# Optimization experiments

Measured on AMD Instinct MI355X. Metric: run time of the kernel, lower is better.

## Reference

```python
import jax, jax.numpy as jnp
import numpy as np


def log_g(x):
    # Appendix B.3 of 'Were RNNs All We Needed?'
    return jnp.where(x >= 0, jnp.log(jax.nn.relu(x) + 0.5), -jax.nn.softplus(-x))


def parallel_scan_log(log_a, log_b):
    # h[0] = b[0]; h[i] = a[i]*h[i-1] + b[i], computed in log space along axis 1
    log_a_star = jnp.cumsum(log_a, axis=1)
    log_x0_plus_b_star = jax.lax.cumlogsumexp(log_b - log_a_star, axis=1)
    return jnp.exp(log_a_star + log_x0_plus_b_star)


def setup_inputs() -> dict:
    key = jax.random.key(0)
    B, T, D = 8, 4096, 1024
    k1, k2, k3, k4, k5 = jax.random.split(key, 5)
    scale = 1.0 / np.sqrt(D)
    return {
        "h_prev_layer": jax.random.normal(k1, (B, T, D), dtype=jnp.float32),
        "W_z": jax.random.uniform(k2, (D, D), jnp.float32, -scale, scale),
        "b_z": jax.random.uniform(k3, (D,), jnp.float32, -scale, scale),
        "W_h": jax.random.uniform(k4, (D, D), jnp.float32, -scale, scale),
        "b_h": jax.random.uniform(k5, (D,), jnp.float32, -scale, scale),
    }


def reference(h_prev_layer, W_z, b_z, W_h, b_h):
    k = jnp.einsum('btd,ed->bte', h_prev_layer, W_z) + b_z          # linear_z
    tilde_h = jnp.einsum('btd,ed->bte', h_prev_layer, W_h) + b_h    # linear_h
    log_z = -jax.nn.softplus(-k)
    log_one_minus_z = -jax.nn.softplus(k)
    log_tilde_h = log_g(tilde_h)
    return parallel_scan_log(log_one_minus_z, log_z + log_tilde_h)
```

## Files before the change

kernel.cpp:

```cpp
#include <hip/hip_runtime.h>
#include <hip/hip_fp16.h>

typedef float f32x4 __attribute__((ext_vector_type(4)));
typedef __bf16 bf16x8 __attribute__((ext_vector_type(8)));

#define BB_ 8
#define TT_ 4096
#define DD_ 1024
#define MM_ (BB_*TT_)
#define KK_ DD_

#define BM 128
#define BN 128
#define BK 32

#define NCH 64
#define LCH (TT_/NCH)

static __device__ __forceinline__ unsigned short f2bf_rn(float f) {
  unsigned int u = __float_as_uint(f);
  u += 0x7FFFu + ((u >> 16) & 1u);
  return (unsigned short)(u >> 16);
}

__global__ void cvt_f32_bf16(const float4* __restrict__ src,
                             ushort4* __restrict__ dst, int n4) {
  int stride = gridDim.x * blockDim.x;
  for (int i = blockIdx.x * blockDim.x + threadIdx.x; i < n4; i += stride) {
    float4 v = src[i];
    ushort4 o;
    o.x = f2bf_rn(v.x); o.y = f2bf_rn(v.y);
    o.z = f2bf_rn(v.z); o.w = f2bf_rn(v.w);
    dst[i] = o;
  }
}

__device__ __forceinline__ void gload_lds16(const void* g, void* l) {
  __builtin_amdgcn_global_load_lds(
      (const __attribute__((address_space(1))) void*)g,
      (__attribute__((address_space(3))) void*)l, 16, 0, 0);
}

__global__ __launch_bounds__(256) void gemm_fused(
    const unsigned short* __restrict__ Xb,
    const unsigned short* __restrict__ Wb,
    const float* __restrict__ bz, const float* __restrict__ bh,
    __half* __restrict__ Zb, __half* __restrict__ Gb)
{
  __shared__ __align__(16) unsigned short lA[BM * BK];
  __shared__ __align__(16) unsigned short lB[BN * BK];
  const int tid  = threadIdx.x;
  const int wave = tid >> 6;
  const int lane = tid & 63;
  const int m0 = blockIdx.x * BM;
  const int e0 = blockIdx.y * BN;
  const int wr = wave >> 1, wc = wave & 1;
  const int fr = lane & 15;
  const int kg = lane >> 4;

  f32x4 acc[4][4];
  #pragma unroll
  for (int i = 0; i < 4; i++)
    #pragma unroll
    for (int j = 0; j < 4; j++)
      acc[i][j] = (f32x4){0.f, 0.f, 0.f, 0.f};

  for (int kk = 0; kk < KK_; kk += BK) {
    #pragma unroll
    for (int it = 0; it < 2; ++it) {
      int il  = (wave * 2 + it) * 64 + lane;
      int row = il >> 2;
      int col = (il & 3) * 8;
      gload_lds16(Xb + (size_t)(m0 + row) * KK_ + kk + col,
                  lA + (size_t)(wave * 2 + it) * 512);
      gload_lds16(Wb + (size_t)(e0 + row) * KK_ + kk + col,
                  lB + (size_t)(wave * 2 + it) * 512);
    }
    __syncthreads();
    bf16x8 af[4], bfv[4];
    #pragma unroll
    for (int i = 0; i < 4; i++)
      af[i] = *reinterpret_cast<const bf16x8*>(&lA[(wr * 64 + i * 16 + fr) * BK + kg * 8]);
    #pragma unroll
    for (int j = 0; j < 4; j++)
      bfv[j] = *reinterpret_cast<const bf16x8*>(&lB[(wc * 64 + j * 16 + fr) * BK + kg * 8]);
    #pragma unroll
    for (int i = 0; i < 4; i++)
      #pragma unroll
      for (int j = 0; j < 4; j++)
        acc[i][j] = __builtin_amdgcn_mfma_f32_16x16x32_bf16(af[i], bfv[j], acc[i][j], 0, 0, 0);
    __syncthreads();
  }

  const bool isZ = (e0 < DD_);
  const float* bias = isZ ? bz : bh;
  __half* outp = isZ ? Zb : Gb;
  const int ec0 = isZ ? e0 : (e0 - DD_);
  #pragma unroll
  for (int j = 0; j < 4; j++) {
    int e = ec0 + wc * 64 + j * 16 + fr;
    float bv = bias[e];
    #pragma unroll
    for (int i = 0; i < 4; i++) {
      int mb = m0 + wr * 64 + i * 16 + kg * 4;
      f32x4 v = acc[i][j];
      #pragma unroll
      for (int r = 0; r < 4; r++) {
        float val = v[r] + bv;
        float res;
        if (isZ) {
          res = 1.0f / (1.0f + __expf(-val));
        } else {
          res = (val >= 0.0f) ? (val + 0.5f)
                              : (1.0f / (1.0f + __expf(-val)));
        }
        outp[(size_t)(mb + r) * DD_ + e] = __float2half(res);
      }
    }
  }
}

__global__ __launch_bounds__(256) void scan_partial(
    const ushort4* __restrict__ Z, const ushort4* __restrict__ G,
    float4* __restrict__ P, float4* __restrict__ Q) {
  const int d4 = threadIdx.x;
  const int c  = blockIdx.x;
  const int b  = blockIdx.y;
  size_t base = ((size_t)b * TT_ + (size_t)c * LCH) * (DD_ / 4) + d4;
  float p0=1.f,p1=1.f,p2=1.f,p3=1.f, q0=0.f,q1=0.f,q2=0.f,q3=0.f;
  for (int t = 0; t < LCH; ++t) {
    ushort4 uz = Z[base + (size_t)t * (DD_ / 4)];
    ushort4 ug = G[base + (size_t)t * (DD_ / 4)];
    float z, g, a;
    z = __half2float(__ushort_as_half(uz.x)); g = __half2float(__ushort_as_half(ug.x));
    a = 1.f - z; p0 *= a; q0 = fmaf(a, q0, z * g);
    z = __half2float(__ushort_as_half(uz.y)); g = __half2float(__ushort_as_half(ug.y));
    a = 1.f - z; p1 *= a; q1 = fmaf(a, q1, z * g);
    z = __half2float(__ushort_as_half(uz.z)); g = __half2float(__ushort_as_half(ug.z));
    a = 1.f - z; p2 *= a; q2 = fmaf(a, q2, z * g);
    z = __half2float(__ushort_as_half(uz.w)); g = __half2float(__ushort_as_half(ug.w));
    a = 1.f - z; p3 *= a; q3 = fmaf(a, q3, z * g);
  }
  size_t o = ((size_t)b * NCH + c) * (DD_ / 4) + d4;
  P[o] = make_float4(p0, p1, p2, p3);
  Q[o] = make_float4(q0, q1, q2, q3);
}

__global__ __launch_bounds__(256) void scan_combine(
    const float4* __restrict__ P, const float4* __restrict__ Q,
    float4* __restrict__ H) {
  const int d4 = threadIdx.x;
  const int b  = blockIdx.x;
  float4 h = make_float4(0.f, 0.f, 0.f, 0.f);
  for (int c = 0; c < NCH; ++c) {
    size_t o = ((size_t)b * NCH + c) * (DD_ / 4) + d4;
    H[o] = h;
    float4 p = P[o], q = Q[o];
    h.x = fmaf(p.x, h.x, q.x);
    h.y = fmaf(p.y, h.y, q.y);
    h.z = fmaf(p.z, h.z, q.z);
    h.w = fmaf(p.w, h.w, q.w);
  }
}

__global__ __launch_bounds__(256) void scan_apply(
    const ushort4* __restrict__ Z, const ushort4* __restrict__ G,
    const float4* __restrict__ H, float4* __restrict__ out) {
  const int d4 = threadIdx.x;
  const int c  = blockIdx.x;
  const int b  = blockIdx.y;
  float4 h = H[((size_t)b * NCH + c) * (DD_ / 4) + d4];
  size_t base = ((size_t)b * TT_ + (size_t)c * LCH) * (DD_ / 4) + d4;
  for (int t = 0; t < LCH; ++t) {
    ushort4 uz = Z[base + (size_t)t * (DD_ / 4)];
    ushort4 ug = G[base + (size_t)t * (DD_ / 4)];
    float z, g, a;
    z = __half2float(__ushort_as_half(uz.x)); g = __half2float(__ushort_as_half(ug.x));
    a = 1.f - z; h.x = fmaf(a, h.x, z * g);
    z = __half2float(__ushort_as_half(uz.y)); g = __half2float(__ushort_as_half(ug.y));
    a = 1.f - z; h.y = fmaf(a, h.y, z * g);
    z = __half2float(__ushort_as_half(uz.z)); g = __half2float(__ushort_as_half(ug.z));
    a = 1.f - z; h.z = fmaf(a, h.z, z * g);
    z = __half2float(__ushort_as_half(uz.w)); g = __half2float(__ushort_as_half(ug.w));
    a = 1.f - z; h.w = fmaf(a, h.w, z * g);
    out[base + (size_t)t * (DD_ / 4)] = h;
  }
}

extern "C" void kernel_launch(void* const* d_in, const int* in_sizes, int n_in,
                              void* d_out, int out_size, void* d_ws, size_t ws_size,
                              hipStream_t stream) {
  const float* X  = (const float*)d_in[0];
  const float* Wz = (const float*)d_in[1];
  const float* bz = (const float*)d_in[2];
  const float* Wh = (const float*)d_in[3];
  const float* bh = (const float*)d_in[4];
  float* out = (float*)d_out;

  const size_t szXb = (size_t)MM_ * DD_ * 2;
  const size_t szWb = (size_t)2 * DD_ * DD_ * 2;
  const size_t szZ  = (size_t)MM_ * DD_ * 2;
  const size_t szPQ = (size_t)BB_ * NCH * DD_ * 4;

  char* ws = (char*)d_ws;
  unsigned short *Xb, *Wb;
  __half *Zb, *Gb;
  const size_t needA = szXb + szWb + 2 * szZ + 3 * szPQ;
  if (ws_size >= needA) {
    Xb = (unsigned short*)ws;              ws += szXb;
    Wb = (unsigned short*)ws;              ws += szWb;
  } else {
    Xb = (unsigned short*)d_out;
    Wb = (unsigned short*)((char*)d_out + szXb);
  }
  Zb = (__half*)ws;  ws += szZ;
  Gb = (__half*)ws;  ws += szZ;
  float* P = (float*)ws;  ws += szPQ;
  float* Q = (float*)ws;  ws += szPQ;
  float* H = (float*)ws;

  cvt_f32_bf16<<<2048, 256, 0, stream>>>((const float4*)X, (ushort4*)Xb,
                                         (int)((size_t)MM_ * DD_ / 4));
  cvt_f32_bf16<<<512, 256, 0, stream>>>((const float4*)Wz, (ushort4*)Wb,
                                        DD_ * DD_ / 4);
  cvt_f32_bf16<<<512, 256, 0, stream>>>((const float4*)Wh,
                                        (ushort4*)(Wb + (size_t)DD_ * DD_),
                                        DD_ * DD_ / 4);
  dim3 gg(MM_ / BM, (2 * DD_) / BN);
  gemm_fused<<<gg, 256, 0, stream>>>(Xb, Wb, bz, bh, Zb, Gb);

  scan_partial<<<dim3(NCH, BB_), 256, 0, stream>>>((const ushort4*)Zb, (const ushort4*)Gb,
                                                   (float4*)P, (float4*)Q);
  scan_combine<<<BB_, 256, 0, stream>>>((const float4*)P, (const float4*)Q, (float4*)H);
  scan_apply<<<dim3(NCH, BB_), 256, 0, stream>>>((const ushort4*)Zb, (const ushort4*)Gb,
                                                 (const float4*)H, (float4*)out);
}
```

Baseline: 325.1 us.

## Double-buffer GEMM LDS tiles, swizzle block order, stage epilogue through LDS

The GEMM main loop now uses two LDS buffers, so the global-to-LDS loads for the next K tile are issued while MFMAs run on the current tile. This removes one barrier per iteration. The grid is flattened with a block-index swizzle that groups tiles sharing rows of X, aiming for better L2 reuse. The epilogue writes fp16 results into LDS first, then stores 16-byte coalesced rows to global memory instead of scattered 2-byte stores. This doubles LDS use to 32KB, which may reduce occupancy.

Measured after the change: 335.3 us. +3.1%, slower.

```diff
diff --git a/kernel.cpp b/kernel.cpp
--- a/kernel.cpp
+++ b/kernel.cpp
@@ -47,16 +47,26 @@
     const float* __restrict__ bz, const float* __restrict__ bh,
     __half* __restrict__ Zb, __half* __restrict__ Gb)
 {
-  __shared__ __align__(16) unsigned short lA[BM * BK];
-  __shared__ __align__(16) unsigned short lB[BN * BK];
+  __shared__ __align__(16) char smem[32768];
+  unsigned short* lA0 = (unsigned short*)(smem);
+  unsigned short* lB0 = (unsigned short*)(smem + 8192);
+  unsigned short* lA1 = (unsigned short*)(smem + 16384);
+  unsigned short* lB1 = (unsigned short*)(smem + 24576);
+
   const int tid  = threadIdx.x;
   const int wave = tid >> 6;
   const int lane = tid & 63;
-  const int m0 = blockIdx.x * BM;
-  const int e0 = blockIdx.y * BN;
+
+  int swz = (blockIdx.x & 7) * 512 + (blockIdx.x >> 3);
+  const int m0 = (swz >> 4) * BM;
+  const int e0 = (swz & 15) * BN;
+
   const int wr = wave >> 1, wc = wave & 1;
   const int fr = lane & 15;
   const int kg = lane >> 4;
+
+  const int il0 = (wave * 2 + 0) * 64 + lane;
+  const int il1 = (wave * 2 + 1) * 64 + lane;
 
   f32x4 acc[4][4];
   #pragma unroll
@@ -65,57 +75,96 @@
     for (int j = 0; j < 4; j++)
       acc[i][j] = (f32x4){0.f, 0.f, 0.f, 0.f};
 
-  for (int kk = 0; kk < KK_; kk += BK) {
-    #pragma unroll
-    for (int it = 0; it < 2; ++it) {
-      int il  = (wave * 2 + it) * 64 + lane;
-      int row = il >> 2;
-      int col = (il & 3) * 8;
-      gload_lds16(Xb + (size_t)(m0 + row) * KK_ + kk + col,
-                  lA + (size_t)(wave * 2 + it) * 512);
-      gload_lds16(Wb + (size_t)(e0 + row) * KK_ + kk + col,
-                  lB + (size_t)(wave * 2 + it) * 512);
-    }
+#define STAGE(dA, dB, kkv) do { \
+    gload_lds16(Xb + (size_t)(m0 + (il0 >> 2)) * KK_ + (kkv) + (il0 & 3) * 8, \
+                (dA) + (size_t)(wave * 2 + 0) * 512); \
+    gload_lds16(Wb + (size_t)(e0 + (il0 >> 2)) * KK_ + (kkv) + (il0 & 3) * 8, \
+                (dB) + (size_t)(wave * 2 + 0) * 512); \
+    gload_lds16(Xb + (size_t)(m0 + (il1 >> 2)) * KK_ + (kkv) + (il1 & 3) * 8, \
+                (dA) + (size_t)(wave * 2 + 1) * 512); \
+    gload_lds16(Wb + (size_t)(e0 + (il1 >> 2)) * KK_ + (kkv) + (il1 & 3) * 8, \
+                (dB) + (size_t)(wave * 2 + 1) * 512); \
+  } while (0)
+
+#define COMPUTE(sA, sB) do { \
+    bf16x8 af[4], bfv[4]; \
+    _Pragma("unroll") \
+    for (int i = 0; i < 4; i++) \
+      af[i] = *reinterpret_cast<const bf16x8*>(&(sA)[(wr * 64 + i * 16 + fr) * BK + kg * 8]); \
+    _Pragma("unroll") \
+    for (int j = 0; j < 4; j++) \
+      bfv[j] = *reinterpret_cast<const bf16x8*>(&(sB)[(wc * 64 + j * 16 + fr) * BK + kg * 8]); \
+    _Pragma("unroll") \
+    for (int i = 0; i < 4; i++) \
+      _Pragma("unroll") \
+      for (int j = 0; j < 4; j++) \
+        acc[i][j] = __builtin_amdgcn_mfma_f32_16x16x32_bf16(af[i], bfv[j], acc[i][j], 0, 0, 0); \
+  } while (0)
+
+  STAGE(lA0, lB0, 0);
+  __syncthreads();
+  int kk = BK;
+  #pragma unroll 1
+  for (int t = 0; t < 15; ++t) {
+    STAGE(lA1, lB1, kk);
+    COMPUTE(lA0, lB0);
     __syncthreads();
-    bf16x8 af[4], bfv[4];
-    #pragma unroll
-    for (int i = 0; i < 4; i++)
-      af[i] = *reinterpret_cast<const bf16x8*>(&lA[(wr * 64 + i * 16 + fr) * BK + kg * 8]);
-    #pragma unroll
-    for (int j = 0; j < 4; j++)
-      bfv[j] = *reinterpret_cast<const bf16x8*>(&lB[(wc * 64 + j * 16 + fr) * BK + kg * 8]);
-    #pragma unroll
-    for (int i = 0; i < 4; i++)
-      #pragma unroll
-      for (int j = 0; j < 4; j++)
-        acc[i][j] = __builtin_amdgcn_mfma_f32_16x16x32_bf16(af[i], bfv[j], acc[i][j], 0, 0, 0);
+    kk += BK;
+    STAGE(lA0, lB0, kk);
+    COMPUTE(lA1, lB1);
     __syncthreads();
-  }
+    kk += BK;
+  }
+  STAGE(lA1, lB1, 31 * BK);
+  COMPUTE(lA0, lB0);
+  __syncthreads();
+  COMPUTE(lA1, lB1);
+  __syncthreads();
+#undef STAGE
+#undef COMPUTE
 
   const bool isZ = (e0 < DD_);
   const float* bias = isZ ? bz : bh;
   __half* outp = isZ ? Zb : Gb;
   const int ec0 = isZ ? e0 : (e0 - DD_);
+
+  float bv[4];
   #pragma unroll
-  for (int j = 0; j < 4; j++) {
-    int e = ec0 + wc * 64 + j * 16 + fr;
-    float bv = bias[e];
+  for (int j = 0; j < 4; j++) bv[j] = bias[ec0 + wc * 64 + j * 16 + fr];
+
+  __half* eo = (__half*)smem;
+  const int sub  = lane & 7;
+  const int rowr = lane >> 3;
+
+  #pragma unroll
+  for (int p = 0; p < 2; ++p) {
     #pragma unroll
-    for (int i = 0; i < 4; i++) {
-      int mb = m0 + wr * 64 + i * 16 + kg * 4;
-      f32x4 v = acc[i][j];
+    for (int i2 = 0; i2 < 2; ++i2) {
+      const int i = p * 2 + i2;
       #pragma unroll
-      for (int r = 0; r < 4; r++) {
-        float val = v[r] + bv;
-        float res;
-        if (isZ) {
-          res = 1.0f / (1.0f + __expf(-val));
-        } else {
-          res = (val >= 0.0f) ? (val + 0.5f)
-                              : (1.0f / (1.0f + __expf(-val)));
+      for (int j = 0; j < 4; j++) {
+        #pragma unroll
+        for (int r = 0; r < 4; r++) {
+          float val = acc[i][j][r] + bv[j];
+          float res;
+          if (isZ) {
+            res = 1.0f / (1.0f + __expf(-val));
+          } else {
+            res = (val >= 0.0f) ? (val + 0.5f)
+                                : (1.0f / (1.0f + __expf(-val)));
+          }
+          eo[(size_t)wave * 2304 + (i2 * 16 + kg * 4 + r) * 72 + j * 16 + fr] =
+              __float2half(res);
         }
-        outp[(size_t)(mb + r) * DD_ + e] = __float2half(res);
       }
+    }
+    #pragma unroll
+    for (int q = 0; q < 4; ++q) {
+      const int rl = q * 8 + rowr;
+      uint4 v = *reinterpret_cast<const uint4*>(
+          &eo[(size_t)wave * 2304 + rl * 72 + sub * 8]);
+      const size_t rg = (size_t)(m0 + wr * 64 + p * 32 + rl);
+      *reinterpret_cast<uint4*>(&outp[rg * DD_ + ec0 + wc * 64 + sub * 8]) = v;
     }
   }
 }
@@ -226,8 +275,7 @@
   cvt_f32_bf16<<<512, 256, 0, stream>>>((const float4*)Wh,
                                         (ushort4*)(Wb + (size_t)DD_ * DD_),
                                         DD_ * DD_ / 4);
-  dim3 gg(MM_ / BM, (2 * DD_) / BN);
-  gemm_fused<<<gg, 256, 0, stream>>>(Xb, Wb, bz, bh, Zb, Gb);
+  gemm_fused<<<(MM_ / BM) * ((2 * DD_) / BN), 256, 0, stream>>>(Xb, Wb, bz, bh, Zb, Gb);
 
   scan_partial<<<dim3(NCH, BB_), 256, 0, stream>>>((const ushort4*)Zb, (const ushort4*)Gb,
                                                    (float4*)P, (float4*)Q);
```

## Rewrite fused GEMM with 256x256 tiles, double-buffered LDS pipeline and swizzled layout

Applied to the files above, without the earlier changes.

The bf16 GEMM moves from 128x128x32 tiles with 256 threads to 256x256x64 tiles with 512 threads. It double-buffers 128 KB of dynamic LDS, interleaving global-to-LDS loads with MFMA phases, and XOR-swizzles the LDS layout to avoid bank conflicts. Blocks are remapped so consecutive blocks share tiles for L2 reuse, and the epilogue stages results through LDS to emit coalesced 16-byte stores. The aim is to cut the GEMM's memory traffic and synchronization stalls, at the cost of higher register and LDS pressure and one block per CU's worth of LDS.

New measurement: 284.3 us. 1.14x faster.

```diff
diff --git a/kernel.cpp b/kernel.cpp
--- a/kernel.cpp
+++ b/kernel.cpp
@@ -9,10 +9,6 @@
 #define DD_ 1024
 #define MM_ (BB_*TT_)
 #define KK_ DD_
-
-#define BM 128
-#define BN 128
-#define BK 32
 
 #define NCH 64
 #define LCH (TT_/NCH)
@@ -41,81 +37,142 @@
       (__attribute__((address_space(3))) void*)l, 16, 0, 0);
 }
 
-__global__ __launch_bounds__(256) void gemm_fused(
+#define STA(q, nb_, kkh) gload_lds16(pXa + (q) * 65536 + (kkh), (nb_) + (q) * 8192 + wofs)
+#define STB(q, nb_, kkh) gload_lds16(pWb + (q) * 65536 + (kkh), (nb_) + 32768 + (q) * 8192 + wofs)
+
+#define PHASE(cb_, mh, kh, STAGEOPS, WAITOPS) do {                          \
+    const char* Ab_ = (cb_);                                                \
+    const char* Bb_ = (cb_) + 32768;                                        \
+    const int sk_ = (kh) ? sk1 : sk0;                                       \
+    bf16x8 af_[4];                                                          \
+    _Pragma("unroll")                                                       \
+    for (int ii = 0; ii < 4; ++ii)                                          \
+      af_[ii] = *reinterpret_cast<const bf16x8*>(                           \
+          Ab_ + rA7 + (mh) * 8192 + ii * 2048 + sk_);                       \
+    if ((mh) == 0) {                                                        \
+      _Pragma("unroll")                                                     \
+      for (int j = 0; j < 4; ++j)                                           \
+        bfv[j] = *reinterpret_cast<const bf16x8*>(                          \
+            Bb_ + rB7 + j * 2048 + sk_);                                    \
+    }                                                                       \
+    STAGEOPS;                                                               \
+    WAITOPS;                                                                \
+    __builtin_amdgcn_s_barrier();                                           \
+    asm volatile("s_waitcnt lgkmcnt(0)" ::: "memory");                      \
+    __builtin_amdgcn_sched_barrier(0);                                      \
+    __builtin_amdgcn_s_setprio(1);                                          \
+    _Pragma("unroll")                                                       \
+    for (int ii = 0; ii < 4; ++ii)                                          \
+      _Pragma("unroll")                                                     \
+      for (int j = 0; j < 4; ++j)                                           \
+        acc[(mh) * 4 + ii][j] = __builtin_amdgcn_mfma_f32_16x16x32_bf16(    \
+            af_[ii], bfv[j], acc[(mh) * 4 + ii][j], 0, 0, 0);               \
+    __builtin_amdgcn_s_setprio(0);                                          \
+    asm volatile("" ::: "memory");                                          \
+    __builtin_amdgcn_s_barrier();                                           \
+  } while (0)
+
+__global__ __launch_bounds__(512, 2) void gemm_fused(
     const unsigned short* __restrict__ Xb,
     const unsigned short* __restrict__ Wb,
     const float* __restrict__ bz, const float* __restrict__ bh,
     __half* __restrict__ Zb, __half* __restrict__ Gb)
 {
-  __shared__ __align__(16) unsigned short lA[BM * BK];
-  __shared__ __align__(16) unsigned short lB[BN * BK];
+  extern __shared__ __align__(16) char smem[];
   const int tid  = threadIdx.x;
   const int wave = tid >> 6;
   const int lane = tid & 63;
-  const int m0 = blockIdx.x * BM;
-  const int e0 = blockIdx.y * BN;
-  const int wr = wave >> 1, wc = wave & 1;
-  const int fr = lane & 15;
-  const int kg = lane >> 4;
-
-  f32x4 acc[4][4];
+  const int wm = wave >> 2, wn = wave & 3;
+  const int fr = lane & 15, kg = lane >> 4, fx = fr & 7;
+
+  int swz = (blockIdx.x & 7) * 128 + (blockIdx.x >> 3);
+  const int m0 = (swz >> 3) * 256;
+  const int e0 = (swz & 7) * 256;
+
+  const int arow = tid >> 3;
+  const int aslx = ((tid & 7) ^ (arow & 7)) * 8;
+  const unsigned short* pXa = Xb + (size_t)(m0 + arow) * KK_ + aslx;
+  const unsigned short* pWb = Wb + (size_t)(e0 + arow) * KK_ + aslx;
+  const int wofs = wave * 1024;
+
+  const int rA7 = (wm * 128 + fr) * 128;
+  const int rB7 = (wn * 64 + fr) * 128;
+  const int sk0 = (kg ^ fx) * 16;
+  const int sk1 = sk0 ^ 64;
+
+  f32x4 acc[8][4];
   #pragma unroll
-  for (int i = 0; i < 4; i++)
+  for (int i = 0; i < 8; i++)
     #pragma unroll
     for (int j = 0; j < 4; j++)
       acc[i][j] = (f32x4){0.f, 0.f, 0.f, 0.f};
-
-  for (int kk = 0; kk < KK_; kk += BK) {
-    #pragma unroll
-    for (int it = 0; it < 2; ++it) {
-      int il  = (wave * 2 + it) * 64 + lane;
-      int row = il >> 2;
-      int col = (il & 3) * 8;
-      gload_lds16(Xb + (size_t)(m0 + row) * KK_ + kk + col,
-                  lA + (size_t)(wave * 2 + it) * 512);
-      gload_lds16(Wb + (size_t)(e0 + row) * KK_ + kk + col,
-                  lB + (size_t)(wave * 2 + it) * 512);
-    }
-    __syncthreads();
-    bf16x8 af[4], bfv[4];
-    #pragma unroll
-    for (int i = 0; i < 4; i++)
-      af[i] = *reinterpret_cast<const bf16x8*>(&lA[(wr * 64 + i * 16 + fr) * BK + kg * 8]);
-    #pragma unroll
-    for (int j = 0; j < 4; j++)
-      bfv[j] = *reinterpret_cast<const bf16x8*>(&lB[(wc * 64 + j * 16 + fr) * BK + kg * 8]);
-    #pragma unroll
-    for (int i = 0; i < 4; i++)
-      #pragma unroll
-      for (int j = 0; j < 4; j++)
-        acc[i][j] = __builtin_amdgcn_mfma_f32_16x16x32_bf16(af[i], bfv[j], acc[i][j], 0, 0, 0);
-    __syncthreads();
+  bf16x8 bfv[4];
+
+  STA(0, smem, 0); STA(2, smem, 0);
+  STB(0, smem, 0); STB(1, smem, 0);
+  STB(2, smem, 0); STB(3, smem, 0);
+  STA(1, smem, 0); STA(3, smem, 0);
+  asm volatile("s_waitcnt vmcnt(2)" ::: "memory");
+  __builtin_amdgcn_s_barrier();
+
+  #pragma unroll 1
+  for (int t = 0; t < 15; ++t) {
+    char* cb = smem + ((t & 1) << 16);
+    char* nb = smem + (((t + 1) & 1) << 16);
+    const int kn = (t + 1) * 64;
+    PHASE(cb, 0, 0, {STA(0, nb, kn); STA(2, nb, kn);},
+          asm volatile("s_waitcnt vmcnt(2)" ::: "memory"));
+    PHASE(cb, 1, 0, {STB(0, nb, kn); STB(1, nb, kn);}, );
+    PHASE(cb, 0, 1, {STB(2, nb, kn); STB(3, nb, kn);}, );
+    PHASE(cb, 1, 1, {STA(1, nb, kn); STA(3, nb, kn);},
+          asm volatile("s_waitcnt vmcnt(2)" ::: "memory"));
+  }
+  {
+    char* cb = smem + 65536;
+    PHASE(cb, 0, 0, {}, asm volatile("s_waitcnt vmcnt(0)" ::: "memory"));
+    PHASE(cb, 1, 0, {}, );
+    PHASE(cb, 0, 1, {}, );
+    PHASE(cb, 1, 1, {}, );
   }
 
   const bool isZ = (e0 < DD_);
   const float* bias = isZ ? bz : bh;
   __half* outp = isZ ? Zb : Gb;
-  const int ec0 = isZ ? e0 : (e0 - DD_);
+  const int ec0 = (isZ ? e0 : (e0 - DD_)) + wn * 64;
+
+  float bv[4];
   #pragma unroll
-  for (int j = 0; j < 4; j++) {
-    int e = ec0 + wc * 64 + j * 16 + fr;
-    float bv = bias[e];
+  for (int j = 0; j < 4; j++) bv[j] = bias[ec0 + j * 16 + fr];
+
+  __half* ew = (__half*)(smem + wave * 9216);
+  const int sub = lane & 7, rowr = lane >> 3;
+
+  #pragma unroll
+  for (int p = 0; p < 2; ++p) {
     #pragma unroll
-    for (int i = 0; i < 4; i++) {
-      int mb = m0 + wr * 64 + i * 16 + kg * 4;
-      f32x4 v = acc[i][j];
+    for (int ii = 0; ii < 4; ++ii) {
       #pragma unroll
-      for (int r = 0; r < 4; r++) {
-        float val = v[r] + bv;
-        float res;
-        if (isZ) {
-          res = 1.0f / (1.0f + __expf(-val));
-        } else {
-          res = (val >= 0.0f) ? (val + 0.5f)
-                              : (1.0f / (1.0f + __expf(-val)));
+      for (int j = 0; j < 4; ++j) {
+        #pragma unroll
+        for (int r = 0; r < 4; ++r) {
+          float val = acc[p * 4 + ii][j][r] + bv[j];
+          float res;
+          if (isZ) {
+            res = 1.0f / (1.0f + __expf(-val));
+          } else {
+            res = (val >= 0.0f) ? (val + 0.5f)
+                                : (1.0f / (1.0f + __expf(-val)));
+          }
+          ew[(ii * 16 + kg * 4 + r) * 72 + j * 16 + fr] = __float2half(res);
         }
-        outp[(size_t)(mb + r) * DD_ + e] = __float2half(res);
       }
+    }
+    #pragma unroll
+    for (int q = 0; q < 8; ++q) {
+      int rl = q * 8 + rowr;
+      uint4 v = *reinterpret_cast<const uint4*>(&ew[rl * 72 + sub * 8]);
+      size_t rg = (size_t)(m0 + wm * 128 + p * 64 + rl);
+      *reinterpret_cast<uint4*>(&outp[rg * DD_ + ec0 + sub * 8]) = v;
     }
   }
 }
@@ -226,8 +283,8 @@
   cvt_f32_bf16<<<512, 256, 0, stream>>>((const float4*)Wh,
                                         (ushort4*)(Wb + (size_t)DD_ * DD_),
                                         DD_ * DD_ / 4);
-  dim3 gg(MM_ / BM, (2 * DD_) / BN);
-  gemm_fused<<<gg, 256, 0, stream>>>(Xb, Wb, bz, bh, Zb, Gb);
+  gemm_fused<<<(MM_ / 256) * ((2 * DD_) / 256), 512, 131072, stream>>>(
+      Xb, Wb, bz, bh, Zb, Gb);
 
   scan_partial<<<dim3(NCH, BB_), 256, 0, stream>>>((const ushort4*)Zb, (const ushort4*)Gb,
                                                    (float4*)P, (float4*)Q);
```
